# Kernel tuning notes

Hardware: AMD Instinct MI355X
Metric: run time of the kernel (lower is better)

## Reference

```python
import jax, jax.numpy as jnp
import numpy as np

ANCHORS = np.array([[10,13],[16,30],[33,23],[30,61],[62,45],[59,119],[116,90],[156,198],[373,326]], dtype=np.float32)
ANCHOR_MASK = [[6,7,8],[3,4,5],[0,1,2]]
NUM_CLASSES = 80
IGNORE_THRESH = 0.5
MAX_BOXES = 32   # fixed padding replacing dynamic boolean-mask box extraction
BS = 16
GRIDS = [13, 26, 52]
NA = 3
INPUT = 416.0


def setup_inputs() -> dict:
    rng = np.random.default_rng(0)
    inp = {}
    for l, g in enumerate(GRIDS):
        inp[f"feats{l}"] = jnp.asarray(rng.normal(0.0, 0.5, size=(BS, NA * (5 + NUM_CLASSES), g, g)).astype(np.float32))
        yt = np.zeros((BS, g, g, NA, 5 + NUM_CLASSES), np.float32)
        n_obj = 20
        for b in range(BS):
            gy = rng.integers(0, g, n_obj); gx = rng.integers(0, g, n_obj); a = rng.integers(0, NA, n_obj)
            yt[b, gy, gx, a, 0:2] = rng.uniform(0.0, 1.0, (n_obj, 2)).astype(np.float32)
            yt[b, gy, gx, a, 2:4] = rng.uniform(0.05, 0.5, (n_obj, 2)).astype(np.float32)
            yt[b, gy, gx, a, 4] = 1.0
            cls = rng.integers(0, NUM_CLASSES, n_obj)
            yt[b, gy, gx, a, 5 + cls] = 1.0
        inp[f"ytrue{l}"] = jnp.asarray(yt)
    return inp


def _bce_logits(x, t):
    # BCEWithLogits (stable): softplus(x) - x*t
    return jax.nn.softplus(x) - x * t


def _pairwise_iou(b1, b2):
    # b1: [bs, N, 4] xywh, b2: [bs, M, 4] xywh -> [bs, N, M]
    b1 = b1[:, :, None, :]
    b2 = b2[:, None, :, :]
    b1_mins = b1[..., :2] - b1[..., 2:4] * 0.5
    b1_maxes = b1[..., :2] + b1[..., 2:4] * 0.5
    b2_mins = b2[..., :2] - b2[..., 2:4] * 0.5
    b2_maxes = b2[..., :2] + b2[..., 2:4] * 0.5
    inter_wh = jnp.clip(jnp.minimum(b1_maxes, b2_maxes) - jnp.maximum(b1_mins, b2_mins), 0.0)
    inter = inter_wh[..., 0] * inter_wh[..., 1]
    a1 = b1[..., 2] * b1[..., 3]
    a2 = b2[..., 2] * b2[..., 3]
    return inter / (a1 + a2 - inter)


def _layer_loss(feats, ytrue, anchors):
    bs, _, gh, gw = feats.shape
    C = 5 + NUM_CLASSES
    raw = feats.reshape(bs, NA, C, gh, gw).transpose(0, 3, 4, 1, 2)  # [bs,gh,gw,na,C]
    gy, gx = jnp.meshgrid(jnp.arange(gh), jnp.arange(gw), indexing="ij")
    grid = jnp.stack([gx, gy], axis=-1).astype(raw.dtype)[None, :, :, None, :]  # [1,gh,gw,1,2] (x,y)
    anchors_t = jnp.asarray(anchors, dtype=raw.dtype)                           # [na,2]
    gshape = jnp.array([gh, gw], raw.dtype)

    pred_xy = (jax.nn.sigmoid(raw[..., :2]) + grid) / gshape
    pred_wh = jnp.exp(raw[..., 2:4]) * anchors_t / INPUT
    pred_box = jnp.concatenate([pred_xy, pred_wh], axis=-1)  # [bs,gh,gw,na,4]

    obj = ytrue[..., 4:5]
    raw_true_xy = ytrue[..., :2] * gshape - grid
    safe_wh = jnp.where(obj > 0, ytrue[..., 2:4], anchors_t / INPUT)  # avoids log(0) off-object
    raw_true_wh = jnp.where(obj > 0, jnp.log(safe_wh / anchors_t * INPUT), 0.0)
    box_loss_scale = 2.0 - ytrue[..., 2:3] * ytrue[..., 3:4]

    # --- best-IoU ignore mask (padded, jit-static replacement for per-image boolean masking) ---
    N = gh * gw * NA
    pb = pred_box.reshape(bs, N, 4)
    obj_flat = obj.reshape(bs, N)
    boxes_flat = ytrue[..., :4].reshape(bs, N, 4)
    vals, idx = jax.lax.top_k(obj_flat, MAX_BOXES)                 # obj cells first
    true_boxes = jnp.take_along_axis(boxes_flat, idx[..., None], axis=1)  # [bs,MAXB,4]
    valid = vals > 0.5                                             # [bs,MAXB]
    iou = jnp.where(valid[:, None, :], _pairwise_iou(pb, true_boxes), 0.0)
    best_iou = jnp.max(iou, axis=2).reshape(bs, gh, gw, NA, 1)
    ignore = (best_iou < IGNORE_THRESH).astype(raw.dtype)

    xy_loss = jnp.sum(obj * box_loss_scale * _bce_logits(raw[..., 0:2], raw_true_xy)) / bs
    wh_loss = jnp.sum(obj * box_loss_scale * jnp.square(raw[..., 2:4] - raw_true_wh)) / bs
    conf_bce = _bce_logits(raw[..., 4:5], obj)
    conf_loss = jnp.sum(conf_bce * obj + (1.0 - obj) * conf_bce * ignore) / bs
    cls_loss = jnp.sum(obj * _bce_logits(raw[..., 5:], ytrue[..., 5:])) / bs
    return xy_loss, wh_loss, conf_loss, cls_loss


def reference(feats0, feats1, feats2, ytrue0, ytrue1, ytrue2):
    feats = [feats0, feats1, feats2]
    ytrue = [ytrue0, ytrue1, ytrue2]
    loss_xy = loss_wh = loss_conf = loss_cls = 0.0
    for l in range(3):
        xy, wh, cf, cl = _layer_loss(feats[l], ytrue[l], ANCHORS[ANCHOR_MASK[l]])
        loss_xy = loss_xy + xy
        loss_wh = loss_wh + wh
        loss_conf = loss_conf + cf
        loss_cls = loss_cls + cl
    total = loss_xy + loss_wh + loss_conf + loss_cls
    return (total[None], loss_xy[None], loss_wh[None], loss_conf[None], loss_cls[None])
```

## Files before the change

### kernel.cpp

```cpp
#include <hip/hip_runtime.h>

#define NCLS 80
#define REC  255
#define NA   3
#define BSZ  16
#define MAXB 32

#define G0 13
#define G1 26
#define G2 52
#define GG0 (G0*G0)
#define GG1 (G1*G1)
#define GG2 (G2*G2)
#define CELLS0 (BSZ*NA*GG0)
#define CELLS1 (BSZ*NA*GG1)
#define CELLS2 (BSZ*NA*GG2)
#define TOTAL  (CELLS0+CELLS1+CELLS2)

#define R0 (BSZ*GG0)
#define R1 (BSZ*GG1)
#define R2 (BSZ*GG2)
#define F0 (R0*REC/4)
#define F1 (R1*REC/4)
#define F2 (R2*REC/4)
#define FT (F0+F1+F2)

#define MB ((TOTAL+255)/256)
#define OB 240

__device__ const float d_anch[3][3][2] = {
  {{116.f, 90.f}, {156.f, 198.f}, {373.f, 326.f}},
  {{ 30.f, 61.f}, { 62.f,  45.f}, { 59.f, 119.f}},
  {{ 10.f, 13.f}, { 16.f,  30.f}, { 33.f,  23.f}},
};

__device__ inline float sp(float x) {
  return fmaxf(x, 0.0f) + log1pf(expf(-fabsf(x)));
}
__device__ inline float sigm(float x) { return 1.0f / (1.0f + expf(-x)); }
__device__ inline float wred(float v) {
  #pragma unroll
  for (int off = 32; off > 0; off >>= 1) v += __shfl_down(v, off, 64);
  return v;
}

template<int L>
__device__ inline void scan4(int q, const float* __restrict__ yt,
                             int* __restrict__ cnt, float* __restrict__ boxes,
                             int* __restrict__ total, int* __restrict__ objlist) {
  constexpr int GG = (L == 0) ? GG0 : (L == 1) ? GG1 : GG2;
  float4 v = ((const float4*)yt)[q];
  float vv[4] = {v.x, v.y, v.z, v.w};
  int w0 = q * 4;
  #pragma unroll
  for (int k = 0; k < 4; ++k) {
    int w = w0 + k;
    unsigned rec = (unsigned)w / 255u;
    int o = w - (int)rec * 255;
    if (o == 4 || o == 89 || o == 174) {
      float obj = vv[k];
      if (obj > 0.5f) {
        int a = (o == 89) ? 1 : (o == 174) ? 2 : 0;
        unsigned b = rec / (unsigned)GG;
        int cell = (int)(rec - b * (unsigned)GG);
        int grp = L * BSZ + (int)b;
        int p = atomicAdd(&cnt[grp], 1);
        if (p < MAXB) {
          const float* rb = yt + (size_t)rec * REC + a * 85;
          float* d = boxes + (grp * MAXB + p) * 4;
          d[0] = rb[0]; d[1] = rb[1]; d[2] = rb[2]; d[3] = rb[3];
        }
        int s = atomicAdd(total, 1);
        if (s < 1024) objlist[s] = (grp << 18) | (a << 16) | cell;
      }
    }
  }
}

__global__ __launch_bounds__(256)
void scan_kernel(const float* __restrict__ y0, const float* __restrict__ y1,
                 const float* __restrict__ y2, int* __restrict__ cnt,
                 float* __restrict__ boxes, int* __restrict__ total,
                 int* __restrict__ objlist) {
  int nth = gridDim.x * blockDim.x;
  for (int q = blockIdx.x * blockDim.x + threadIdx.x; q < FT; q += nth) {
    if (q < F0)           scan4<0>(q,           y0, cnt, boxes, total, objlist);
    else if (q < F0 + F1) scan4<1>(q - F0,      y1, cnt, boxes, total, objlist);
    else                  scan4<2>(q - F0 - F1, y2, cnt, boxes, total, objlist);
  }
}

__device__ inline float best_iou(float px, float py, float pw, float ph,
                                 const float* __restrict__ boxes, int grp, int nb) {
  float pminx = px - pw * 0.5f, pmaxx = px + pw * 0.5f;
  float pminy = py - ph * 0.5f, pmaxy = py + ph * 0.5f;
  float pa = pw * ph;
  const float4* bxs = (const float4*)(boxes + grp * MAXB * 4);
  float best = 0.0f;
  for (int j = 0; j < nb; ++j) {
    float4 tb = bxs[j];
    float iw = fminf(pmaxx, tb.x + tb.z * 0.5f) - fmaxf(pminx, tb.x - tb.z * 0.5f);
    float ih = fminf(pmaxy, tb.y + tb.w * 0.5f) - fmaxf(pminy, tb.y - tb.w * 0.5f);
    iw = fmaxf(iw, 0.f); ih = fmaxf(ih, 0.f);
    float inter = iw * ih;
    best = fmaxf(best, inter / (pa + tb.z * tb.w - inter));
  }
  return best;
}

template<int L>
__device__ inline float conf_cell(int idx, const float* __restrict__ fp,
                                  const int* __restrict__ cnt,
                                  const float* __restrict__ boxes) {
  constexpr int GG = (L == 0) ? GG0 : (L == 1) ? GG1 : GG2;
  constexpr int G  = (L == 0) ? G0  : (L == 1) ? G1  : G2;
  unsigned rest = (unsigned)idx / (unsigned)GG;
  int cell = idx - (int)rest * GG;
  unsigned b = rest / 3u;
  int a = (int)(rest - b * 3u);
  int fbase = ((int)(b * 3u) + a) * 85 * GG + cell;
  float t0 = fp[fbase];
  float t1 = fp[fbase + GG];
  float t2 = fp[fbase + 2 * GG];
  float t3 = fp[fbase + 3 * GG];
  float t4 = fp[fbase + 4 * GG];
  unsigned yi = (unsigned)cell / (unsigned)G;
  int xi = cell - (int)yi * G;
  float inv_g = 1.0f / (float)G;
  float aw = d_anch[L][a][0], ah = d_anch[L][a][1];
  float px = (sigm(t0) + (float)xi) * inv_g;
  float py = (sigm(t1) + (float)yi) * inv_g;
  float pw = expf(t2) * aw * (1.0f / 416.0f);
  float ph = expf(t3) * ah * (1.0f / 416.0f);
  int grp = L * BSZ + (int)b;
  int nb = cnt[grp]; nb = nb > MAXB ? MAXB : nb;
  float best = best_iou(px, py, pw, ph, boxes, grp, nb);
  return sp(t4) * (best < 0.5f ? 1.0f : 0.0f);
}

__global__ __launch_bounds__(256)
void loss_kernel(const float* __restrict__ f0, const float* __restrict__ f1,
                 const float* __restrict__ f2, const float* __restrict__ y0,
                 const float* __restrict__ y1, const float* __restrict__ y2,
                 const int* __restrict__ cnt, const float* __restrict__ boxes,
                 const int* __restrict__ total, const int* __restrict__ objlist,
                 float* __restrict__ acc, int* __restrict__ done,
                 float* __restrict__ out) {
  float vxy = 0.f, vwh = 0.f, vconf = 0.f, vcls = 0.f;
  int lane = threadIdx.x & 63, wv = threadIdx.x >> 6;

  if (blockIdx.x < MB) {
    int t = blockIdx.x * 256 + threadIdx.x;
    if (t < TOTAL) {
      if (t < CELLS0)                vconf = conf_cell<0>(t,                  f0, cnt, boxes);
      else if (t < CELLS0 + CELLS1)  vconf = conf_cell<1>(t - CELLS0,         f1, cnt, boxes);
      else                           vconf = conf_cell<2>(t - CELLS0 - CELLS1, f2, cnt, boxes);
    }
  } else {
    int e = (blockIdx.x - MB) * 4 + wv;
    int tot = *total; if (tot > 1024) tot = 1024;
    if (e < tot) {
      int pk = objlist[e];
      int grp = pk >> 18, a = (pk >> 16) & 3, cell = pk & 0xFFFF;
      int l = grp >> 4, b = grp & 15;
      int GGv, Gv;
      const float *fp, *yp;
      if (l == 0)      { GGv = GG0; Gv = G0; fp = f0; yp = y0; }
      else if (l == 1) { GGv = GG1; Gv = G1; fp = f1; yp = y1; }
      else             { GGv = GG2; Gv = G2; fp = f2; yp = y2; }
      int rec   = b * GGv + cell;
      int ybase = rec * REC + a * 85;
      int fbase = (b * NA + a) * 85 * GGv + cell;
      float objv = yp[ybase + 4];

      {
        float lg = fp[fbase + (5 + lane) * GGv];
        vcls = sp(lg) - lg * yp[ybase + 5 + lane];
        if (lane < 16) {
          int c2 = lane + 64;
          float lg2 = fp[fbase + (5 + c2) * GGv];
          vcls += sp(lg2) - lg2 * yp[ybase + 5 + c2];
        }
        vcls *= objv;
      }

      if (lane == 0) {
        float t0 = fp[fbase];
        float t1 = fp[fbase + GGv];
        float t2 = fp[fbase + 2 * GGv];
        float t3 = fp[fbase + 3 * GGv];
        float t4 = fp[fbase + 4 * GGv];
        float ytx = yp[ybase], yty = yp[ybase + 1];
        float ytw = yp[ybase + 2], yth = yp[ybase + 3];
        int yi = cell / Gv, xi = cell - yi * Gv;
        float aw = d_anch[l][a][0], ah = d_anch[l][a][1];
        float rtx = ytx * (float)Gv - (float)xi;
        float rty = yty * (float)Gv - (float)yi;
        float scale = 2.0f - ytw * yth;
        vxy = objv * scale * ((sp(t0) - t0 * rtx) + (sp(t1) - t1 * rty));
        float rtw = logf(ytw * 416.0f / aw);
        float rth = logf(yth * 416.0f / ah);
        vwh = objv * scale * ((t2 - rtw) * (t2 - rtw) + (t3 - rth) * (t3 - rth));
        float px = (sigm(t0) + (float)xi) / (float)Gv;
        float py = (sigm(t1) + (float)yi) / (float)Gv;
        float pw = expf(t2) * aw * (1.0f / 416.0f);
        float ph = expf(t3) * ah * (1.0f / 416.0f);
        int nb = cnt[grp]; nb = nb > MAXB ? MAXB : nb;
        float best = best_iou(px, py, pw, ph, boxes, grp, nb);
        float ign = best < 0.5f ? 1.0f : 0.0f;
        float spt4 = sp(t4);
        float bce4 = spt4 - t4 * objv;
        vconf = bce4 * (objv + (1.0f - objv) * ign) - spt4 * ign;
      }
    }
  }

  __shared__ float sm[4][4];
  vxy = wred(vxy); vwh = wred(vwh); vconf = wred(vconf); vcls = wred(vcls);
  if (lane == 0) { sm[0][wv] = vxy; sm[1][wv] = vwh; sm[2][wv] = vconf; sm[3][wv] = vcls; }
  __syncthreads();
  if (threadIdx.x < 4) {
    float s = sm[threadIdx.x][0] + sm[threadIdx.x][1] + sm[threadIdx.x][2] + sm[threadIdx.x][3];
    atomicAdd(&acc[threadIdx.x], s);
  }
  __syncthreads();

  if (threadIdx.x == 0) {
    __threadfence();
    int d = atomicAdd(done, 1);
    if (d == (int)gridDim.x - 1) {
      float xy = atomicAdd(&acc[0], 0.0f) * (1.0f / BSZ);
      float wh = atomicAdd(&acc[1], 0.0f) * (1.0f / BSZ);
      float cf = atomicAdd(&acc[2], 0.0f) * (1.0f / BSZ);
      float cl = atomicAdd(&acc[3], 0.0f) * (1.0f / BSZ);
      out[0] = xy + wh + cf + cl;
      out[1] = xy; out[2] = wh; out[3] = cf; out[4] = cl;
    }
  }
}

extern "C" void kernel_launch(void* const* d_in, const int* in_sizes, int n_in,
                              void* d_out, int out_size, void* d_ws, size_t ws_size,
                              hipStream_t stream) {
  const float* f0 = (const float*)d_in[0];
  const float* y0 = (const float*)d_in[1];
  const float* f1 = (const float*)d_in[2];
  const float* y1 = (const float*)d_in[3];
  const float* f2 = (const float*)d_in[4];
  const float* y2 = (const float*)d_in[5];

  float* acc     = (float*)d_ws;
  int*   cnt     = (int*)((char*)d_ws + 64);
  int*   total   = (int*)((char*)d_ws + 256);
  int*   done    = (int*)((char*)d_ws + 260);
  int*   objlist = (int*)((char*)d_ws + 512);
  float* boxes   = (float*)((char*)d_ws + 8192);

  hipMemsetAsync(d_ws, 0, 512, stream);

  scan_kernel<<<2048, 256, 0, stream>>>(y0, y1, y2, cnt, boxes, total, objlist);
  loss_kernel<<<MB + OB, 256, 0, stream>>>(f0, f1, f2, y0, y1, y2,
                                           cnt, boxes, total, objlist,
                                           acc, done, (float*)d_out);
}
```

Measured before the change: 167.0 us.

## Gather objectness only, stage boxes in LDS, parallelize object IoU across lanes

The first kernel stops streaming the entire ytrue tensor as float4 and instead uses one thread per cell/anchor to read only the objectness value (plus the box when an object is present). This removes most of the ytrue read traffic from the scan. The conf pass now preloads each block's ground-truth boxes and counts into shared memory before the IoU loop. The object path spreads the IoU over lanes with a wave max reduction instead of looping serially on lane 0. The gather reads are strided by 85 floats, so they are uncoalesced and may waste part of each fetched cache line.

```diff
diff --git a/kernel.cpp b/kernel.cpp
--- a/kernel.cpp
+++ b/kernel.cpp
@@ -17,14 +17,6 @@
 #define CELLS2 (BSZ*NA*GG2)
 #define TOTAL  (CELLS0+CELLS1+CELLS2)
 
-#define R0 (BSZ*GG0)
-#define R1 (BSZ*GG1)
-#define R2 (BSZ*GG2)
-#define F0 (R0*REC/4)
-#define F1 (R1*REC/4)
-#define F2 (R2*REC/4)
-#define FT (F0+F1+F2)
-
 #define MB ((TOTAL+255)/256)
 #define OB 240
 
@@ -43,75 +35,60 @@
   for (int off = 32; off > 0; off >>= 1) v += __shfl_down(v, off, 64);
   return v;
 }
+__device__ inline float wmax(float v) {
+  #pragma unroll
+  for (int off = 32; off > 0; off >>= 1) v = fmaxf(v, __shfl_xor(v, off, 64));
+  return v;
+}
+
+__device__ inline int cell_grp(int t) {
+  if (t < CELLS0) {
+    unsigned r = (unsigned)t / (unsigned)GG0; return (int)(r / 3u);
+  } else if (t < CELLS0 + CELLS1) {
+    unsigned r = (unsigned)(t - CELLS0) / (unsigned)GG1; return 16 + (int)(r / 3u);
+  }
+  unsigned r = (unsigned)(t - CELLS0 - CELLS1) / (unsigned)GG2; return 32 + (int)(r / 3u);
+}
 
 template<int L>
-__device__ inline void scan4(int q, const float* __restrict__ yt,
-                             int* __restrict__ cnt, float* __restrict__ boxes,
-                             int* __restrict__ total, int* __restrict__ objlist) {
+__device__ inline void gather_one(int idx, const float* __restrict__ yt,
+                                  int* __restrict__ cnt, float* __restrict__ boxes,
+                                  int* __restrict__ total, int* __restrict__ objlist) {
   constexpr int GG = (L == 0) ? GG0 : (L == 1) ? GG1 : GG2;
-  float4 v = ((const float4*)yt)[q];
-  float vv[4] = {v.x, v.y, v.z, v.w};
-  int w0 = q * 4;
-  #pragma unroll
-  for (int k = 0; k < 4; ++k) {
-    int w = w0 + k;
-    unsigned rec = (unsigned)w / 255u;
-    int o = w - (int)rec * 255;
-    if (o == 4 || o == 89 || o == 174) {
-      float obj = vv[k];
-      if (obj > 0.5f) {
-        int a = (o == 89) ? 1 : (o == 174) ? 2 : 0;
-        unsigned b = rec / (unsigned)GG;
-        int cell = (int)(rec - b * (unsigned)GG);
-        int grp = L * BSZ + (int)b;
-        int p = atomicAdd(&cnt[grp], 1);
-        if (p < MAXB) {
-          const float* rb = yt + (size_t)rec * REC + a * 85;
-          float* d = boxes + (grp * MAXB + p) * 4;
-          d[0] = rb[0]; d[1] = rb[1]; d[2] = rb[2]; d[3] = rb[3];
-        }
-        int s = atomicAdd(total, 1);
-        if (s < 1024) objlist[s] = (grp << 18) | (a << 16) | cell;
-      }
-    }
+  unsigned rest = (unsigned)idx / (unsigned)GG;
+  int cell = idx - (int)rest * GG;
+  unsigned b = rest / 3u;
+  int a = (int)(rest - b * 3u);
+  size_t base = ((size_t)((int)b * GG + cell) * 3 + a) * 85;
+  float obj = yt[base + 4];
+  if (obj > 0.5f) {
+    int grp = L * BSZ + (int)b;
+    int p = atomicAdd(&cnt[grp], 1);
+    if (p < MAXB) {
+      float* d = boxes + (grp * MAXB + p) * 4;
+      d[0] = yt[base]; d[1] = yt[base + 1]; d[2] = yt[base + 2]; d[3] = yt[base + 3];
+    }
+    int s = atomicAdd(total, 1);
+    if (s < 1024) objlist[s] = (grp << 18) | (a << 16) | cell;
   }
 }
 
 __global__ __launch_bounds__(256)
-void scan_kernel(const float* __restrict__ y0, const float* __restrict__ y1,
-                 const float* __restrict__ y2, int* __restrict__ cnt,
-                 float* __restrict__ boxes, int* __restrict__ total,
-                 int* __restrict__ objlist) {
-  int nth = gridDim.x * blockDim.x;
-  for (int q = blockIdx.x * blockDim.x + threadIdx.x; q < FT; q += nth) {
-    if (q < F0)           scan4<0>(q,           y0, cnt, boxes, total, objlist);
-    else if (q < F0 + F1) scan4<1>(q - F0,      y1, cnt, boxes, total, objlist);
-    else                  scan4<2>(q - F0 - F1, y2, cnt, boxes, total, objlist);
-  }
-}
-
-__device__ inline float best_iou(float px, float py, float pw, float ph,
-                                 const float* __restrict__ boxes, int grp, int nb) {
-  float pminx = px - pw * 0.5f, pmaxx = px + pw * 0.5f;
-  float pminy = py - ph * 0.5f, pmaxy = py + ph * 0.5f;
-  float pa = pw * ph;
-  const float4* bxs = (const float4*)(boxes + grp * MAXB * 4);
-  float best = 0.0f;
-  for (int j = 0; j < nb; ++j) {
-    float4 tb = bxs[j];
-    float iw = fminf(pmaxx, tb.x + tb.z * 0.5f) - fmaxf(pminx, tb.x - tb.z * 0.5f);
-    float ih = fminf(pmaxy, tb.y + tb.w * 0.5f) - fmaxf(pminy, tb.y - tb.w * 0.5f);
-    iw = fmaxf(iw, 0.f); ih = fmaxf(ih, 0.f);
-    float inter = iw * ih;
-    best = fmaxf(best, inter / (pa + tb.z * tb.w - inter));
-  }
-  return best;
+void gather_kernel(const float* __restrict__ y0, const float* __restrict__ y1,
+                   const float* __restrict__ y2, int* __restrict__ cnt,
+                   float* __restrict__ boxes, int* __restrict__ total,
+                   int* __restrict__ objlist) {
+  int t = blockIdx.x * 256 + threadIdx.x;
+  if (t >= TOTAL) return;
+  if (t < CELLS0)               gather_one<0>(t,                   y0, cnt, boxes, total, objlist);
+  else if (t < CELLS0 + CELLS1) gather_one<1>(t - CELLS0,          y1, cnt, boxes, total, objlist);
+  else                          gather_one<2>(t - CELLS0 - CELLS1, y2, cnt, boxes, total, objlist);
 }
 
 template<int L>
 __device__ inline float conf_cell(int idx, const float* __restrict__ fp,
-                                  const int* __restrict__ cnt,
-                                  const float* __restrict__ boxes) {
+                                  const float4* __restrict__ sbox,
+                                  const int* __restrict__ scnt, int gmin) {
   constexpr int GG = (L == 0) ? GG0 : (L == 1) ? GG1 : GG2;
   constexpr int G  = (L == 0) ? G0  : (L == 1) ? G1  : G2;
   unsigned rest = (unsigned)idx / (unsigned)GG;
@@ -132,9 +109,21 @@
   float py = (sigm(t1) + (float)yi) * inv_g;
   float pw = expf(t2) * aw * (1.0f / 416.0f);
   float ph = expf(t3) * ah * (1.0f / 416.0f);
-  int grp = L * BSZ + (int)b;
-  int nb = cnt[grp]; nb = nb > MAXB ? MAXB : nb;
-  float best = best_iou(px, py, pw, ph, boxes, grp, nb);
+  int si = L * BSZ + (int)b - gmin;
+  int nb = scnt[si]; nb = nb > MAXB ? MAXB : nb;
+  const float4* bx = sbox + si * MAXB;
+  float pminx = px - pw * 0.5f, pmaxx = px + pw * 0.5f;
+  float pminy = py - ph * 0.5f, pmaxy = py + ph * 0.5f;
+  float pa = pw * ph;
+  float best = 0.0f;
+  for (int j = 0; j < nb; ++j) {
+    float4 tb = bx[j];
+    float iw = fminf(pmaxx, tb.x + tb.z * 0.5f) - fmaxf(pminx, tb.x - tb.z * 0.5f);
+    float ih = fminf(pmaxy, tb.y + tb.w * 0.5f) - fmaxf(pminy, tb.y - tb.w * 0.5f);
+    iw = fmaxf(iw, 0.f); ih = fmaxf(ih, 0.f);
+    float inter = iw * ih;
+    best = fmaxf(best, inter / (pa + tb.z * tb.w - inter));
+  }
   return sp(t4) * (best < 0.5f ? 1.0f : 0.0f);
 }
 
@@ -146,15 +135,25 @@
                  const int* __restrict__ total, const int* __restrict__ objlist,
                  float* __restrict__ acc, int* __restrict__ done,
                  float* __restrict__ out) {
+  __shared__ float4 sbox[2 * MAXB];
+  __shared__ int scnt[2];
   float vxy = 0.f, vwh = 0.f, vconf = 0.f, vcls = 0.f;
   int lane = threadIdx.x & 63, wv = threadIdx.x >> 6;
 
   if (blockIdx.x < MB) {
-    int t = blockIdx.x * 256 + threadIdx.x;
+    int tfirst = blockIdx.x * 256;
+    int tlast  = min(tfirst + 255, TOTAL - 1);
+    int gmin = cell_grp(tfirst);
+    int ng = cell_grp(tlast) - gmin + 1;
+    if (threadIdx.x < ng * MAXB)
+      sbox[threadIdx.x] = ((const float4*)boxes)[gmin * MAXB + threadIdx.x];
+    if (threadIdx.x < ng) scnt[threadIdx.x] = cnt[gmin + threadIdx.x];
+    __syncthreads();
+    int t = tfirst + threadIdx.x;
     if (t < TOTAL) {
-      if (t < CELLS0)                vconf = conf_cell<0>(t,                  f0, cnt, boxes);
-      else if (t < CELLS0 + CELLS1)  vconf = conf_cell<1>(t - CELLS0,         f1, cnt, boxes);
-      else                           vconf = conf_cell<2>(t - CELLS0 - CELLS1, f2, cnt, boxes);
+      if (t < CELLS0)                vconf = conf_cell<0>(t,                   f0, sbox, scnt, gmin);
+      else if (t < CELLS0 + CELLS1)  vconf = conf_cell<1>(t - CELLS0,          f1, sbox, scnt, gmin);
+      else                           vconf = conf_cell<2>(t - CELLS0 - CELLS1, f2, sbox, scnt, gmin);
     }
   } else {
     int e = (blockIdx.x - MB) * 4 + wv;
@@ -173,27 +172,41 @@
       int fbase = (b * NA + a) * 85 * GGv + cell;
       float objv = yp[ybase + 4];
 
-      {
-        float lg = fp[fbase + (5 + lane) * GGv];
-        vcls = sp(lg) - lg * yp[ybase + 5 + lane];
-        if (lane < 16) {
-          int c2 = lane + 64;
-          float lg2 = fp[fbase + (5 + c2) * GGv];
-          vcls += sp(lg2) - lg2 * yp[ybase + 5 + c2];
-        }
-        vcls *= objv;
+      float lg = fp[fbase + (5 + lane) * GGv];
+      vcls = sp(lg) - lg * yp[ybase + 5 + lane];
+      if (lane < 16) {
+        int c2 = lane + 64;
+        float lg2 = fp[fbase + (5 + c2) * GGv];
+        vcls += sp(lg2) - lg2 * yp[ybase + 5 + c2];
       }
-
+      vcls *= objv;
+
+      float t0 = fp[fbase];
+      float t1 = fp[fbase + GGv];
+      float t2 = fp[fbase + 2 * GGv];
+      float t3 = fp[fbase + 3 * GGv];
+      float t4 = fp[fbase + 4 * GGv];
+      int yi = (l == 0) ? cell / G0 : (l == 1) ? cell / G1 : cell / G2;
+      int xi = cell - yi * Gv;
+      float aw = d_anch[l][a][0], ah = d_anch[l][a][1];
+      float px = (sigm(t0) + (float)xi) / (float)Gv;
+      float py = (sigm(t1) + (float)yi) / (float)Gv;
+      float pw = expf(t2) * aw * (1.0f / 416.0f);
+      float ph = expf(t3) * ah * (1.0f / 416.0f);
+      int nb = cnt[grp]; nb = nb > MAXB ? MAXB : nb;
+      float iou = 0.0f;
+      if (lane < nb) {
+        float4 tb = ((const float4*)boxes)[grp * MAXB + lane];
+        float iw = fminf(px + pw * 0.5f, tb.x + tb.z * 0.5f) - fmaxf(px - pw * 0.5f, tb.x - tb.z * 0.5f);
+        float ih = fminf(py + ph * 0.5f, tb.y + tb.w * 0.5f) - fmaxf(py - ph * 0.5f, tb.y - tb.w * 0.5f);
+        iw = fmaxf(iw, 0.f); ih = fmaxf(ih, 0.f);
+        float inter = iw * ih;
+        iou = inter / (pw * ph + tb.z * tb.w - inter);
+      }
+      float best = wmax(iou);
       if (lane == 0) {
-        float t0 = fp[fbase];
-        float t1 = fp[fbase + GGv];
-        float t2 = fp[fbase + 2 * GGv];
-        float t3 = fp[fbase + 3 * GGv];
-        float t4 = fp[fbase + 4 * GGv];
         float ytx = yp[ybase], yty = yp[ybase + 1];
         float ytw = yp[ybase + 2], yth = yp[ybase + 3];
-        int yi = cell / Gv, xi = cell - yi * Gv;
-        float aw = d_anch[l][a][0], ah = d_anch[l][a][1];
         float rtx = ytx * (float)Gv - (float)xi;
         float rty = yty * (float)Gv - (float)yi;
         float scale = 2.0f - ytw * yth;
@@ -201,12 +214,6 @@
         float rtw = logf(ytw * 416.0f / aw);
         float rth = logf(yth * 416.0f / ah);
         vwh = objv * scale * ((t2 - rtw) * (t2 - rtw) + (t3 - rth) * (t3 - rth));
-        float px = (sigm(t0) + (float)xi) / (float)Gv;
-        float py = (sigm(t1) + (float)yi) / (float)Gv;
-        float pw = expf(t2) * aw * (1.0f / 416.0f);
-        float ph = expf(t3) * ah * (1.0f / 416.0f);
-        int nb = cnt[grp]; nb = nb > MAXB ? MAXB : nb;
-        float best = best_iou(px, py, pw, ph, boxes, grp, nb);
         float ign = best < 0.5f ? 1.0f : 0.0f;
         float spt4 = sp(t4);
         float bce4 = spt4 - t4 * objv;
@@ -258,7 +265,7 @@
 
   hipMemsetAsync(d_ws, 0, 512, stream);
 
-  scan_kernel<<<2048, 256, 0, stream>>>(y0, y1, y2, cnt, boxes, total, objlist);
+  gather_kernel<<<MB, 256, 0, stream>>>(y0, y1, y2, cnt, boxes, total, objlist);
   loss_kernel<<<MB + OB, 256, 0, stream>>>(f0, f1, f2, y0, y1, y2,
                                            cnt, boxes, total, objlist,
                                            acc, done, (float*)d_out);
```

After: 171.6 us. +2.7%, slower.
